# Kernel optimization log

Measured on AMD Instinct MI355X. Metric: run time of the kernel, lower is better.

Reference implementation:

```python
import jax, jax.numpy as jnp
import numpy as np

B, T, D, K = 32, 2048, 1024, 31


def setup_inputs() -> dict:
    key = jax.random.key(0)
    ks = jax.random.split(key, 8)
    query = jax.random.normal(ks[0], (B, D), dtype=jnp.float32)
    memory = jax.random.normal(ks[1], (B, T, D), dtype=jnp.float32)
    prev_attn = jax.nn.softmax(jax.random.normal(ks[2], (B, T)), axis=-1).astype(jnp.float32)
    cum_attn = jax.random.uniform(ks[3], (B, T), dtype=jnp.float32)
    mask = jax.random.bernoulli(ks[4], 0.2, (B, T))
    mask = mask.at[:, 0].set(False)  # keep at least one valid position per row
    scale = 0.02
    Wq = jax.random.normal(ks[5], (D, D), dtype=jnp.float32) * scale    # torch Linear weight [out,in]
    Wm = jax.random.normal(ks[6], (D, D), dtype=jnp.float32) * scale
    k2 = jax.random.split(ks[7], 2)
    Wloc = jax.random.normal(k2[0], (D, 2, K), dtype=jnp.float32) * scale  # Conv1d weight [out_ch,in_ch,k]
    v = jax.random.normal(k2[1], (D,), dtype=jnp.float32) * scale          # Linear(d_model,1) weight squeezed
    return {"query": query, "memory": memory, "prev_attn": prev_attn,
            "cum_attn": cum_attn, "mask": mask,
            "Wq": Wq, "Wm": Wm, "Wloc": Wloc, "v": v}


def reference(query, memory, prev_attn, cum_attn, mask, Wq, Wm, Wloc, v):
    pad = Wloc.shape[-1] // 2
    # location features: [B,2,T] conv -> [B,D,T] -> [B,T,D]
    loc_in = jnp.stack([prev_attn, cum_attn], axis=1)
    loc = jax.lax.conv_general_dilated(
        loc_in, Wloc, window_strides=(1,), padding=[(pad, pad)],
        dimension_numbers=("NCW", "OIW", "NCW"))
    loc = jnp.transpose(loc, (0, 2, 1))                 # [B,T,D]
    q = (query @ Wq.T)[:, None, :]                      # [B,1,D]
    m = jnp.einsum("btd,ed->bte", memory, Wm)           # [B,T,D]
    e = jnp.einsum("btd,d->bt", jnp.tanh(q + m + loc), v)  # [B,T]
    e = jnp.where(mask, -jnp.inf, e)
    a = jax.nn.softmax(e, axis=1)                       # [B,T]
    ctx = jnp.einsum("bt,btd->bd", a, memory)           # [B,D]
    return ctx, a
```

## Files before the change

### kernel.cpp

```cpp
#include <hip/hip_runtime.h>
#include <math.h>

#define BATCH 32
#define T 2048
#define D 1024
#define KW 31
#define CPAD 15
#define KEXT 62
#define KTOT 1088
#define BM 128
#define BN 128
#define BK 32
#define NSTEP (KTOT / BK)

typedef __bf16 bf16_8 __attribute__((ext_vector_type(8)));
typedef __bf16 bf16_4 __attribute__((ext_vector_type(4)));
typedef float  f32x4  __attribute__((ext_vector_type(4)));

__device__ __forceinline__ float tanh_fast(float x) {
    return 1.f - 2.f * __builtin_amdgcn_rcpf(__expf(2.f * x) + 1.f);
}

__device__ __forceinline__ void glds16(const void* gsrc, void* ldst) {
    __builtin_amdgcn_global_load_lds(
        (const __attribute__((address_space(1))) unsigned int*)gsrc,
        (__attribute__((address_space(3))) unsigned int*)ldst, 16, 0, 0);
}

__global__ __launch_bounds__(256) void k_prep_b(const float* __restrict__ Wm,
                                                const float* __restrict__ Wloc,
                                                __bf16* __restrict__ Bext) {
    const int idx = blockIdx.x * 256 + threadIdx.x;
    const int d = idx / (KTOT / 4);
    const int kk = (idx % (KTOT / 4)) * 4;
    bf16_4 o;
    #pragma unroll
    for (int u = 0; u < 4; ++u) {
        const int k = kk + u;
        float val = 0.f;
        if (k < D) val = Wm[(size_t)d * D + k];
        else {
            const int j = k - D;
            if (j < KEXT) {
                const int c = (j >= KW) ? 1 : 0;
                const int kp = j - c * KW;
                val = Wloc[((size_t)d * 2 + c) * KW + kp];
            }
        }
        o[u] = (__bf16)val;
    }
    *(bf16_4*)(Bext + (size_t)d * KTOT + kk) = o;
}

__global__ __launch_bounds__(256) void k_prep_amem(const float* __restrict__ memory,
                                                   __bf16* __restrict__ Amem) {
    const int nvec = BATCH * T * (D / 16);
    for (int idx = blockIdx.x * 256 + threadIdx.x; idx < nvec; idx += gridDim.x * 256) {
        const int row = idx >> 6;
        const int c = (idx & 63) * 16;
        const float* src = memory + (size_t)row * D + c;
        const f32x4 a0 = *(const f32x4*)(src);
        const f32x4 a1 = *(const f32x4*)(src + 4);
        const f32x4 a2 = *(const f32x4*)(src + 8);
        const f32x4 a3 = *(const f32x4*)(src + 12);
        bf16_8 o0, o1;
        #pragma unroll
        for (int u = 0; u < 4; ++u) {
            o0[u] = (__bf16)a0[u]; o0[u + 4] = (__bf16)a1[u];
            o1[u] = (__bf16)a2[u]; o1[u + 4] = (__bf16)a3[u];
        }
        __bf16* dst = Amem + (size_t)row * KTOT + c;
        *(bf16_8*)(dst) = o0;
        *(bf16_8*)(dst + 8) = o1;
    }
}

__global__ __launch_bounds__(256) void k_prep_aloc(const float* __restrict__ prev,
                                                   const float* __restrict__ cum,
                                                   __bf16* __restrict__ Amem) {
    const int idx = blockIdx.x * 256 + threadIdx.x;
    const int row = idx >> 4;
    const int j0 = (idx & 15) * 4;
    const int b = row >> 11;
    const int t = row & (T - 1);
    bf16_4 o;
    #pragma unroll
    for (int u = 0; u < 4; ++u) {
        const int j = j0 + u;
        float val = 0.f;
        if (j < KEXT) {
            const int c = (j >= KW) ? 1 : 0;
            const int kp = j - c * KW;
            const int ts = t + kp - CPAD;
            if (ts >= 0 && ts < T)
                val = (c ? cum : prev)[(size_t)b * T + ts];
        }
        o[u] = (__bf16)val;
    }
    *(bf16_4*)(Amem + (size_t)row * KTOT + D + j0) = o;
}

__global__ __launch_bounds__(256) void k_q(const float* __restrict__ query,
                                           const float* __restrict__ Wq,
                                           float* __restrict__ qout) {
    int b = blockIdx.y;
    int w = threadIdx.x >> 6;
    int lane = threadIdx.x & 63;
    int d = blockIdx.x * 4 + w;
    const float* qrow = query + (size_t)b * D;
    const float* wrow = Wq + (size_t)d * D;
    float s = 0.f;
    #pragma unroll
    for (int i = 0; i < D / 64; ++i) s += qrow[lane + i * 64] * wrow[lane + i * 64];
    #pragma unroll
    for (int off = 32; off > 0; off >>= 1) s += __shfl_down(s, off, 64);
    if (lane == 0) qout[(size_t)b * D + d] = s;
}

__global__ __launch_bounds__(256, 4) void k_gemm_e(
    const __bf16* __restrict__ Amem, const __bf16* __restrict__ Bext,
    const float* __restrict__ qv, const float* __restrict__ vvec,
    float* __restrict__ e_part) {
    __shared__ bf16_8 As[3][512];
    __shared__ bf16_8 Bs[2][512];

    const int t0 = blockIdx.x * BM;
    const int d0 = blockIdx.y * BN;
    const int b  = blockIdx.z;
    const int tid  = threadIdx.x;
    const int lane = tid & 63;
    const int w    = tid >> 6;
    const int wr   = w >> 1, wc = w & 1;
    const int q    = lane >> 4, m = lane & 15;

    f32x4 acc[4][4] = {};

    const int g0 = w, g1 = w + 4;
    const __bf16* aptr0 = Amem + ((size_t)b * T + t0 + g0 * 16 + m) * KTOT + q * 8;
    const __bf16* aptr1 = Amem + ((size_t)b * T + t0 + g1 * 16 + m) * KTOT + q * 8;
    const __bf16* bptr0 = Bext + (size_t)(d0 + g0 * 16 + m) * KTOT + q * 8;
    const __bf16* bptr1 = Bext + (size_t)(d0 + g1 * 16 + m) * KTOT + q * 8;

    auto compute = [&](int pA, int pB) {
        bf16_8 bfr[4];
        #pragma unroll
        for (int j = 0; j < 4; ++j) bfr[j] = Bs[pB][(wc * 4 + j) * 64 + lane];
        #pragma unroll
        for (int i = 0; i < 4; ++i) {
            const bf16_8 af = As[pA][(wr * 4 + i) * 64 + lane];
            #pragma unroll
            for (int j = 0; j < 4; ++j)
                acc[i][j] = __builtin_amdgcn_mfma_f32_16x16x32_bf16(af, bfr[j], acc[i][j], 0, 0, 0);
        }
    };

    glds16(aptr0,      &As[0][g0 * 64]);
    glds16(aptr1,      &As[0][g1 * 64]);
    glds16(bptr0,      &Bs[0][g0 * 64]);
    glds16(bptr1,      &Bs[0][g1 * 64]);
    glds16(aptr0 + BK, &As[1][g0 * 64]);
    glds16(aptr1 + BK, &As[1][g1 * 64]);

    #pragma unroll 1
    for (int k = 0; k < NSTEP - 1; ++k) {
        asm volatile("s_waitcnt vmcnt(2)" ::: "memory");
        __builtin_amdgcn_s_barrier();
        const int kb1 = k + 1;
        glds16(bptr0 + kb1 * BK, &Bs[kb1 & 1][g0 * 64]);
        glds16(bptr1 + kb1 * BK, &Bs[kb1 & 1][g1 * 64]);
        const int ka2 = k + 2;
        if (ka2 < NSTEP) {
            glds16(aptr0 + ka2 * BK, &As[ka2 % 3][g0 * 64]);
            glds16(aptr1 + ka2 * BK, &As[ka2 % 3][g1 * 64]);
        }
        compute(k % 3, k & 1);
    }
    asm volatile("s_waitcnt vmcnt(0)" ::: "memory");
    __builtin_amdgcn_s_barrier();
    compute((NSTEP - 1) % 3, (NSTEP - 1) & 1);

    float qreg[4], vreg[4];
    #pragma unroll
    for (int j = 0; j < 4; ++j) {
        const int d = d0 + wc * 64 + j * 16 + m;
        qreg[j] = qv[(size_t)b * D + d];
        vreg[j] = vvec[d];
    }
    const int dch = blockIdx.y * 2 + wc;
    #pragma unroll
    for (int i = 0; i < 4; ++i) {
        #pragma unroll
        for (int r = 0; r < 4; ++r) {
            float s = 0.f;
            #pragma unroll
            for (int j = 0; j < 4; ++j)
                s += tanh_fast(acc[i][j][r] + qreg[j]) * vreg[j];
            #pragma unroll
            for (int off = 8; off > 0; off >>= 1)
                s += __shfl_down(s, off, 16);
            if (m == 0) {
                const int t = t0 + wr * 64 + i * 16 + q * 4 + r;
                e_part[((size_t)b * T + t) * 16 + dch] = s;
            }
        }
    }
}

__global__ __launch_bounds__(256) void k_softmax(const float* __restrict__ e_part,
                                                 const int* __restrict__ mask,
                                                 float* __restrict__ aout) {
    const int b = blockIdx.x;
    const int tid = threadIdx.x;
    __shared__ float red[256];
    float ev[8];
    float lmax = -INFINITY;
    #pragma unroll
    for (int i = 0; i < 8; ++i) {
        const int t = tid + i * 256;
        const float* p = e_part + ((size_t)b * T + t) * 16;
        float s = 0.f;
        #pragma unroll
        for (int c = 0; c < 16; ++c) s += p[c];
        if (mask[(size_t)b * T + t] != 0) s = -INFINITY;
        ev[i] = s;
        lmax = fmaxf(lmax, s);
    }
    red[tid] = lmax; __syncthreads();
    for (int off = 128; off > 0; off >>= 1) {
        if (tid < off) red[tid] = fmaxf(red[tid], red[tid + off]);
        __syncthreads();
    }
    const float mx = red[0]; __syncthreads();
    float lsum = 0.f;
    #pragma unroll
    for (int i = 0; i < 8; ++i) {
        const float x = expf(ev[i] - mx);
        ev[i] = x;
        lsum += x;
    }
    red[tid] = lsum; __syncthreads();
    for (int off = 128; off > 0; off >>= 1) {
        if (tid < off) red[tid] += red[tid + off];
        __syncthreads();
    }
    const float inv = 1.f / red[0];
    #pragma unroll
    for (int i = 0; i < 8; ++i)
        aout[(size_t)b * T + tid + i * 256] = ev[i] * inv;
}

__global__ __launch_bounds__(256) void k_ctx_part(const float* __restrict__ memory,
                                                  const float* __restrict__ a,
                                                  float* __restrict__ ctx_part) {
    const int b = blockIdx.x;
    const int tc = blockIdx.y;
    const int d4 = threadIdx.x * 4;
    f32x4 acc = {0.f, 0.f, 0.f, 0.f};
    const float* mb = memory + ((size_t)b * T + (size_t)tc * 64) * D;
    const float* ab = a + (size_t)b * T + (size_t)tc * 64;
    #pragma unroll 4
    for (int t = 0; t < 64; ++t) {
        const float wgt = ab[t];
        const f32x4 m4 = *(const f32x4*)(mb + (size_t)t * D + d4);
        acc += wgt * m4;
    }
    *(f32x4*)(ctx_part + ((size_t)(b * 32 + tc)) * D + d4) = acc;
}

__global__ __launch_bounds__(256) void k_ctx_red(const float* __restrict__ ctx_part,
                                                 float* __restrict__ ctx) {
    const int idx = blockIdx.x * 256 + threadIdx.x;
    const int b = idx >> 10, d = idx & 1023;
    float s = 0.f;
    #pragma unroll
    for (int tc = 0; tc < 32; ++tc) s += ctx_part[((size_t)(b * 32 + tc)) * D + d];
    ctx[idx] = s;
}

extern "C" void kernel_launch(void* const* d_in, const int* in_sizes, int n_in,
                              void* d_out, int out_size, void* d_ws, size_t ws_size,
                              hipStream_t stream) {
    const float* query  = (const float*)d_in[0];
    const float* memory = (const float*)d_in[1];
    const float* prev   = (const float*)d_in[2];
    const float* cum    = (const float*)d_in[3];
    const int*   mask   = (const int*)d_in[4];
    const float* Wq     = (const float*)d_in[5];
    const float* Wm     = (const float*)d_in[6];
    const float* Wloc   = (const float*)d_in[7];
    const float* v      = (const float*)d_in[8];

    float* out = (float*)d_out;
    float* ctx = out;
    float* a   = out + BATCH * D;

    char* ws = (char*)d_ws;
    float*  qv       = (float*)(ws + 0);
    float*  e_part   = (float*)(ws + 131072);
    float*  ctx_part = (float*)(ws + 4325376);
    __bf16* Bext     = (__bf16*)(ws + 8519680);
    __bf16* Amem     = (__bf16*)(ws + 10747904);

    k_prep_b<<<KTOT * D / (256 * 4), 256, 0, stream>>>(Wm, Wloc, Bext);
    k_prep_amem<<<4096, 256, 0, stream>>>(memory, Amem);
    k_prep_aloc<<<BATCH * T * 16 / 256, 256, 0, stream>>>(prev, cum, Amem);
    k_q<<<dim3(D / 4, BATCH), 256, 0, stream>>>(query, Wq, qv);
    k_gemm_e<<<dim3(T / BM, D / BN, BATCH), 256, 0, stream>>>(Amem, Bext, qv, v, e_part);
    k_softmax<<<BATCH, 256, 0, stream>>>(e_part, mask, a);
    k_ctx_part<<<dim3(BATCH, 32), 256, 0, stream>>>(memory, a, ctx_part);
    k_ctx_red<<<(BATCH * D) / 256, 256, 0, stream>>>(ctx_part, ctx);
}
```

Baseline: 729.0 us.

## Enlarge GEMM tile to 256x256 with 8 waves and quarter-split pipelined staging

The fused energy GEMM moves from 128x128 tiles with 4 waves to 256x256 tiles with 8 waves and a K step of 64. Each K iteration is split into four quarter MFMA phases, with the async global-to-LDS loads for the next stage interleaved between them and s_setprio raising wave priority around the MFMA blocks. The larger tile increases operand reuse and cuts global traffic per FLOP. In exchange it uses 128 KB of LDS per block and more registers, which lowers occupancy, and it adds more barriers. The e_part chunk index now counts 4 column groups per block, matching the 16 partial slots the softmax expects.

```diff
diff --git a/kernel.cpp b/kernel.cpp
--- a/kernel.cpp
+++ b/kernel.cpp
@@ -8,10 +8,10 @@
 #define CPAD 15
 #define KEXT 62
 #define KTOT 1088
-#define BM 128
-#define BN 128
-#define BK 32
-#define NSTEP (KTOT / BK)
+#define BM 256
+#define BN 256
+#define KSTEP 64
+#define NK (KTOT / KSTEP)
 
 typedef __bf16 bf16_8 __attribute__((ext_vector_type(8)));
 typedef __bf16 bf16_4 __attribute__((ext_vector_type(4)));
@@ -26,6 +26,12 @@
         (const __attribute__((address_space(1))) unsigned int*)gsrc,
         (__attribute__((address_space(3))) unsigned int*)ldst, 16, 0, 0);
 }
+
+#define VM4 asm volatile("s_waitcnt vmcnt(4)" ::: "memory")
+#define VM0 asm volatile("s_waitcnt vmcnt(0)" ::: "memory")
+#define BAR __builtin_amdgcn_s_barrier()
+#define PRIO1 __builtin_amdgcn_s_setprio(1)
+#define PRIO0 __builtin_amdgcn_s_setprio(0)
 
 __global__ __launch_bounds__(256) void k_prep_b(const float* __restrict__ Wm,
                                                 const float* __restrict__ Wloc,
@@ -117,12 +123,12 @@
     if (lane == 0) qout[(size_t)b * D + d] = s;
 }
 
-__global__ __launch_bounds__(256, 4) void k_gemm_e(
+__global__ __launch_bounds__(512, 2) void k_gemm_e(
     const __bf16* __restrict__ Amem, const __bf16* __restrict__ Bext,
     const float* __restrict__ qv, const float* __restrict__ vvec,
     float* __restrict__ e_part) {
-    __shared__ bf16_8 As[3][512];
-    __shared__ bf16_8 Bs[2][512];
+    __shared__ bf16_8 As[2][2048];
+    __shared__ bf16_8 Bs[2][2048];
 
     const int t0 = blockIdx.x * BM;
     const int d0 = blockIdx.y * BN;
@@ -130,76 +136,128 @@
     const int tid  = threadIdx.x;
     const int lane = tid & 63;
     const int w    = tid >> 6;
-    const int wr   = w >> 1, wc = w & 1;
-    const int q    = lane >> 4, m = lane & 15;
-
-    f32x4 acc[4][4] = {};
-
-    const int g0 = w, g1 = w + 4;
-    const __bf16* aptr0 = Amem + ((size_t)b * T + t0 + g0 * 16 + m) * KTOT + q * 8;
-    const __bf16* aptr1 = Amem + ((size_t)b * T + t0 + g1 * 16 + m) * KTOT + q * 8;
-    const __bf16* bptr0 = Bext + (size_t)(d0 + g0 * 16 + m) * KTOT + q * 8;
-    const __bf16* bptr1 = Bext + (size_t)(d0 + g1 * 16 + m) * KTOT + q * 8;
-
-    auto compute = [&](int pA, int pB) {
-        bf16_8 bfr[4];
-        #pragma unroll
-        for (int j = 0; j < 4; ++j) bfr[j] = Bs[pB][(wc * 4 + j) * 64 + lane];
-        #pragma unroll
-        for (int i = 0; i < 4; ++i) {
-            const bf16_8 af = As[pA][(wr * 4 + i) * 64 + lane];
-            #pragma unroll
-            for (int j = 0; j < 4; ++j)
-                acc[i][j] = __builtin_amdgcn_mfma_f32_16x16x32_bf16(af, bfr[j], acc[i][j], 0, 0, 0);
-        }
-    };
-
-    glds16(aptr0,      &As[0][g0 * 64]);
-    glds16(aptr1,      &As[0][g1 * 64]);
-    glds16(bptr0,      &Bs[0][g0 * 64]);
-    glds16(bptr1,      &Bs[0][g1 * 64]);
-    glds16(aptr0 + BK, &As[1][g0 * 64]);
-    glds16(aptr1 + BK, &As[1][g1 * 64]);
+    const int wm   = w >> 2;
+    const int wn   = w & 3;
+    const int ml   = lane & 15;
+    const int qk   = lane >> 4;
+
+    f32x4 acc[8][4] = {};
+
+    const __bf16* gA[2][2];
+    const __bf16* gB[2][2];
+    int sA[2][2], sB[2][2];
+    #pragma unroll
+    for (int h = 0; h < 2; ++h) {
+        #pragma unroll
+        for (int j = 0; j < 2; ++j) {
+            const int idx = j * 8 + w;
+            const int p = idx >> 1, kfa = idx & 1;
+            const int mf = h * 4 + (p & 3) + (idx & 8);
+            const int nf = h * 2 + (p & 1) + (p >> 1) * 4;
+            gA[h][j] = Amem + ((size_t)b * T + t0 + mf * 16 + ml) * KTOT + kfa * 32 + qk * 8;
+            sA[h][j] = (mf * 2 + kfa) * 64;
+            gB[h][j] = Bext + (size_t)(d0 + nf * 16 + ml) * KTOT + kfa * 32 + qk * 8;
+            sB[h][j] = (nf * 2 + kfa) * 64;
+        }
+    }
+
+    bf16_8 areg[4][2];
+    bf16_8 breg0[2][2], breg1[2][2];
+
+    auto STG_A = [&](int h, int kcol, bf16_8* dst) {
+        glds16(gA[h][0] + kcol, dst + sA[h][0]);
+        glds16(gA[h][1] + kcol, dst + sA[h][1]);
+    };
+    auto STG_B = [&](int h, int kcol, bf16_8* dst) {
+        glds16(gB[h][0] + kcol, dst + sB[h][0]);
+        glds16(gB[h][1] + kcol, dst + sB[h][1]);
+    };
+    auto LDA = [&](const bf16_8* buf, int ih) {
+        #pragma unroll
+        for (int i = 0; i < 4; ++i)
+            #pragma unroll
+            for (int kf = 0; kf < 2; ++kf)
+                areg[i][kf] = buf[((wm * 8 + ih * 4 + i) * 2 + kf) * 64 + lane];
+    };
+    auto LDB = [&](bf16_8 (&dst)[2][2], const bf16_8* buf, int jh) {
+        #pragma unroll
+        for (int j = 0; j < 2; ++j)
+            #pragma unroll
+            for (int kf = 0; kf < 2; ++kf)
+                dst[j][kf] = buf[((wn * 4 + jh * 2 + j) * 2 + kf) * 64 + lane];
+    };
+    auto QMM = [&](bf16_8 (&bb)[2][2], int ih, int jh) {
+        #pragma unroll
+        for (int i = 0; i < 4; ++i)
+            #pragma unroll
+            for (int kf = 0; kf < 2; ++kf)
+                #pragma unroll
+                for (int j = 0; j < 2; ++j)
+                    acc[ih * 4 + i][jh * 2 + j] = __builtin_amdgcn_mfma_f32_16x16x32_bf16(
+                        areg[i][kf], bb[j][kf], acc[ih * 4 + i][jh * 2 + j], 0, 0, 0);
+    };
+
+    STG_A(0, 0, As[0]);
+    STG_B(0, 0, Bs[0]);
+    STG_B(1, 0, Bs[0]);
+    STG_A(1, 0, As[0]);
+    VM4;
+    BAR;
 
     #pragma unroll 1
-    for (int k = 0; k < NSTEP - 1; ++k) {
-        asm volatile("s_waitcnt vmcnt(2)" ::: "memory");
-        __builtin_amdgcn_s_barrier();
-        const int kb1 = k + 1;
-        glds16(bptr0 + kb1 * BK, &Bs[kb1 & 1][g0 * 64]);
-        glds16(bptr1 + kb1 * BK, &Bs[kb1 & 1][g1 * 64]);
-        const int ka2 = k + 2;
-        if (ka2 < NSTEP) {
-            glds16(aptr0 + ka2 * BK, &As[ka2 % 3][g0 * 64]);
-            glds16(aptr1 + ka2 * BK, &As[ka2 % 3][g1 * 64]);
-        }
-        compute(k % 3, k & 1);
-    }
-    asm volatile("s_waitcnt vmcnt(0)" ::: "memory");
-    __builtin_amdgcn_s_barrier();
-    compute((NSTEP - 1) % 3, (NSTEP - 1) & 1);
+    for (int k = 0; k < NK; ++k) {
+        const bf16_8* Ac = As[k & 1];
+        const bf16_8* Bc = Bs[k & 1];
+        bf16_8* An = As[(k + 1) & 1];
+        bf16_8* Bn = Bs[(k + 1) & 1];
+        const int c1 = ((k + 1 < NK) ? (k + 1) : 0) * KSTEP;
+        LDA(Ac, 0);
+        LDB(breg0, Bc, 0);
+        STG_A(0, c1, An);
+        BAR;
+        PRIO1; QMM(breg0, 0, 0); PRIO0;
+        VM4;
+        BAR;
+        LDB(breg1, Bc, 1);
+        STG_B(0, c1, Bn);
+        BAR;
+        PRIO1; QMM(breg1, 0, 1); PRIO0;
+        VM4;
+        BAR;
+        LDA(Ac, 1);
+        STG_B(1, c1, Bn);
+        BAR;
+        PRIO1; QMM(breg0, 1, 0); PRIO0;
+        BAR;
+        STG_A(1, c1, An);
+        BAR;
+        PRIO1; QMM(breg1, 1, 1); PRIO0;
+        VM4;
+        BAR;
+    }
+    VM0;
 
     float qreg[4], vreg[4];
     #pragma unroll
-    for (int j = 0; j < 4; ++j) {
-        const int d = d0 + wc * 64 + j * 16 + m;
-        qreg[j] = qv[(size_t)b * D + d];
-        vreg[j] = vvec[d];
-    }
-    const int dch = blockIdx.y * 2 + wc;
-    #pragma unroll
-    for (int i = 0; i < 4; ++i) {
+    for (int jb = 0; jb < 4; ++jb) {
+        const int d = d0 + wn * 64 + jb * 16 + ml;
+        qreg[jb] = qv[(size_t)b * D + d];
+        vreg[jb] = vvec[d];
+    }
+    const int dch = blockIdx.y * 4 + wn;
+    #pragma unroll
+    for (int ia = 0; ia < 8; ++ia) {
         #pragma unroll
         for (int r = 0; r < 4; ++r) {
             float s = 0.f;
             #pragma unroll
-            for (int j = 0; j < 4; ++j)
-                s += tanh_fast(acc[i][j][r] + qreg[j]) * vreg[j];
+            for (int jb = 0; jb < 4; ++jb)
+                s += tanh_fast(acc[ia][jb][r] + qreg[jb]) * vreg[jb];
             #pragma unroll
             for (int off = 8; off > 0; off >>= 1)
                 s += __shfl_down(s, off, 16);
-            if (m == 0) {
-                const int t = t0 + wr * 64 + i * 16 + q * 4 + r;
+            if (ml == 0) {
+                const int t = t0 + wm * 128 + ia * 16 + qk * 4 + r;
                 e_part[((size_t)b * T + t) * 16 + dch] = s;
             }
         }
@@ -305,7 +363,7 @@
     k_prep_amem<<<4096, 256, 0, stream>>>(memory, Amem);
     k_prep_aloc<<<BATCH * T * 16 / 256, 256, 0, stream>>>(prev, cum, Amem);
     k_q<<<dim3(D / 4, BATCH), 256, 0, stream>>>(query, Wq, qv);
-    k_gemm_e<<<dim3(T / BM, D / BN, BATCH), 256, 0, stream>>>(Amem, Bext, qv, v, e_part);
+    k_gemm_e<<<dim3(T / BM, D / BN, BATCH), 512, 0, stream>>>(Amem, Bext, qv, v, e_part);
     k_softmax<<<BATCH, 256, 0, stream>>>(e_part, mask, a);
     k_ctx_part<<<dim3(BATCH, 32), 256, 0, stream>>>(memory, a, ctx_part);
     k_ctx_red<<<(BATCH * D) / 256, 256, 0, stream>>>(ctx_part, ctx);
```

After: 686.1 us. -5.9%, faster.
